# Optimization experiments

Measured on AMD Instinct MI355X. Metric: run time of the kernel, lower is better.

## Reference

```python
import jax, jax.numpy as jnp
import numpy as np

NUM_ATOMS = 100000
NUM_BONDS = 200000
MAX_NB = 6
ATOM_FDIM = 133
BOND_FDIM = 147
HIDDEN = 300
READOUT = 512
DEPTH = 6
ATOMS_PER_MOL = 25
NUM_MOLS = NUM_ATOMS // ATOMS_PER_MOL


def setup_inputs() -> dict:
    key = jax.random.key(0)
    ks = jax.random.split(key, 16)
    s = 0.02
    inp = {
        "f_atoms": jax.random.normal(ks[0], (NUM_ATOMS, ATOM_FDIM), jnp.float32),
        "f_bonds": jax.random.normal(ks[1], (NUM_BONDS, BOND_FDIM), jnp.float32),
        "a2b": jax.random.randint(ks[2], (NUM_ATOMS, MAX_NB), 0, NUM_BONDS),
        "b2a": jax.random.randint(ks[3], (NUM_BONDS,), 0, NUM_ATOMS),
        "b2revb": jax.random.randint(ks[4], (NUM_BONDS,), 0, NUM_BONDS),
        "mol_id": jnp.arange(NUM_ATOMS) // ATOMS_PER_MOL,
        # parameters (Linear: y = x @ W + b)
        "W_i": jax.random.normal(ks[5], (BOND_FDIM, HIDDEN), jnp.float32) * s,
        "b_i": jnp.zeros((HIDDEN,), jnp.float32),
        "W_h": jax.random.normal(ks[6], (HIDDEN, HIDDEN), jnp.float32) * s,
        "b_h": jnp.zeros((HIDDEN,), jnp.float32),
        "W_o": jax.random.normal(ks[7], (ATOM_FDIM + HIDDEN, HIDDEN), jnp.float32) * s,
        "b_o": jnp.zeros((HIDDEN,), jnp.float32),
        "W_fc0": jax.random.normal(ks[8], (HIDDEN, READOUT), jnp.float32) * s,
        "b_fc0": jnp.zeros((READOUT,), jnp.float32),
        "W_fc1": jax.random.normal(ks[9], (READOUT, READOUT), jnp.float32) * s,
        "b_fc1": jnp.zeros((READOUT,), jnp.float32),
        "W_last": jax.random.normal(ks[10], (READOUT, 1), jnp.float32) * s,
        "b_last": jnp.zeros((1,), jnp.float32),
    }
    return inp


def reference(f_atoms, f_bonds, W_i, b_i, W_h, b_h, W_o, b_o,
              W_fc0, b_fc0, W_fc1, b_fc1, W_last, b_last,
              a2b, b2a, b2revb, mol_id):
    relu = jax.nn.relu
    # input = W_i(f_bonds); message = relu(input)  (dropout p=0 -> identity)
    inp = f_bonds @ W_i + b_i                      # [B, H]
    message = relu(inp)
    for _ in range(DEPTH - 1):
        nei = message[a2b]                          # [A, nb, H] gather
        a_message = nei.sum(axis=1)                 # [A, H]
        rev_message = message[b2revb]               # [B, H]
        message = a_message[b2a] - rev_message      # [B, H]
        message = relu(inp + (message @ W_h + b_h))
    # final atom aggregation
    a_message = message[a2b].sum(axis=1)            # [A, H]
    a_input = jnp.concatenate([f_atoms, a_message], axis=1)
    atom_hiddens = relu(a_input @ W_o + b_o)        # [A, H]
    # molecule mean-pool (a_scope -> segment mean over mol_id)
    sums = jax.ops.segment_sum(atom_hiddens, mol_id, num_segments=NUM_MOLS)
    counts = jax.ops.segment_sum(jnp.ones((atom_hiddens.shape[0], 1), atom_hiddens.dtype),
                                 mol_id, num_segments=NUM_MOLS)
    mol_vecs = sums / jnp.maximum(counts, 1.0)      # [M, H]
    # readout MLP
    h = relu(mol_vecs @ W_fc0 + b_fc0)
    h = relu(h @ W_fc1 + b_fc1)
    out = h @ W_last + b_last                       # [M, 1]
    return out.reshape(-1)
```

## Files before the change

kernel.cpp:

```cpp
#include <hip/hip_runtime.h>

#define NATOMS 100000
#define NBONDS 200000
#define NMOLS  4000

typedef __bf16 bf16x8 __attribute__((ext_vector_type(8)));
typedef float  f32x4  __attribute__((ext_vector_type(4)));

__device__ unsigned short g_packWi [5  * 40 * 512];
__device__ unsigned short g_packWh [10 * 40 * 512];
__device__ unsigned short g_packWoT[5  * 40 * 512];
__device__ unsigned short g_packWoB[10 * 40 * 512];

__device__ __forceinline__ float bf2f(unsigned short u) {
    union { unsigned int i; float f; } c; c.i = ((unsigned int)u) << 16; return c.f;
}
__device__ __forceinline__ unsigned short f2bf(float f) {
    union { float f; unsigned int i; } c; c.f = f;
    unsigned int r = (c.i + 0x7FFFu + ((c.i >> 16) & 1u)) >> 16;
    return (unsigned short)r;
}
__device__ __forceinline__ unsigned int relu2(unsigned int u) {
    if (u & 0x00008000u) u &= 0xFFFF0000u;
    if (u & 0x80000000u) u &= 0x0000FFFFu;
    return u;
}

__global__ void pack_weights(const float* __restrict__ W_i,
                             const float* __restrict__ W_h,
                             const float* __restrict__ W_o)
{
    const int gid = blockIdx.x * blockDim.x + threadIdx.x;
    if (gid >= 1200 * 512) return;
    const int gg = gid >> 9;
    const int t  = gid & 511;
    const float* src; int K; unsigned short* dst; int lg;
    if (gg < 200)      { lg = gg;       src = W_i;             K = 147; dst = g_packWi; }
    else if (gg < 600) { lg = gg - 200; src = W_h;             K = 300; dst = g_packWh; }
    else if (gg < 800) { lg = gg - 600; src = W_o;             K = 133; dst = g_packWoT; }
    else               { lg = gg - 800; src = W_o + 133 * 300; K = 300; dst = g_packWoB; }
    const int s = lg / 40, r = lg % 40;
    const int f = r >> 1, hl = r & 1;
    const int ln = t >> 3, j = t & 7;
    const int k = 32 * s + 8 * (ln >> 4) + j;
    const int n = 16 * f + (ln & 15);
    float val = (k < K && n < 300) ? src[k * 300 + n] : 0.f;
    unsigned short hi = f2bf(val);
    dst[(long)lg * 512 + t] = hl ? f2bf(val - bf2f(hi)) : hi;
}

__global__ __launch_bounds__(512)
void gemm_mfma6(const void* __restrict__ Ap, int a16, int sel,
                const float* __restrict__ bias, const float* __restrict__ Cin,
                void* __restrict__ outR, int r16,
                unsigned short* __restrict__ outP16,
                long M, int K, int ksteps, int do_relu)
{
    __shared__ unsigned long long lds8[98304 / 8];
    unsigned short* Asm = (unsigned short*)lds8;
    unsigned short* Bsm = (unsigned short*)lds8 + 8192;
    unsigned short* ep  = (unsigned short*)lds8;

    const unsigned short* pp =
        (sel == 0) ? g_packWi : (sel == 1) ? g_packWh :
        (sel == 2) ? g_packWoT : g_packWoB;

    const int tid = threadIdx.x;
    const int wv  = tid >> 6;
    const int ln  = tid & 63;
    const int l15 = ln & 15;
    const int g   = ln >> 4;
    const int wm  = wv >> 2;
    const int wn  = wv & 3;
    const long row0 = (long)blockIdx.x * 128;

    f32x4 acc[4][5];
#pragma unroll
    for (int m = 0; m < 4; ++m)
#pragma unroll
        for (int f = 0; f < 5; ++f) acc[m][f] = (f32x4){0.f, 0.f, 0.f, 0.f};

    int aoff[4];
#pragma unroll
    for (int m = 0; m < 4; ++m) {
        const int r = wm * 64 + m * 16 + l15;
        aoff[m] = r * 32 + 8 * (g ^ ((r >> 1) & 3));
    }

    const int srow = tid >> 2, sq = tid & 3;
    const int sqs  = sq ^ ((srow >> 1) & 3);

#define STAGE_A(BUF, SS)                                                       \
    do {                                                                       \
        if (a16) {                                                             \
            const char* src = (const char*)Ap +                                \
                (row0 + srow) * (size_t)600 + (SS) * 64 + sqs * 16;            \
            char* dst = (char*)Asm + (BUF) * 8192 + srow * 64 + sq * 16;       \
            __builtin_amdgcn_global_load_lds(                                  \
                (const __attribute__((address_space(1))) void*)src,            \
                (__attribute__((address_space(3))) void*)dst, 16, 0, 0);       \
        } else {                                                               \
            const float* A = (const float*)Ap;                                 \
            const long gr = row0 + srow;                                       \
            const int kb = (SS) * 32 + sqs * 8;                                \
            unsigned short tv[8];                                              \
            _Pragma("unroll")                                                  \
            for (int e = 0; e < 8; ++e)                                        \
                tv[e] = (gr < M && kb + e < K) ? f2bf(A[gr * (long)K + kb + e]) \
                                               : (unsigned short)0;            \
            ushort4 w0 = {tv[0], tv[1], tv[2], tv[3]};                         \
            ushort4 w1 = {tv[4], tv[5], tv[6], tv[7]};                         \
            *(ushort4*)(Asm + (BUF) * 4096 + srow * 32 + sq * 8)     = w0;     \
            *(ushort4*)(Asm + (BUF) * 4096 + srow * 32 + sq * 8 + 4) = w1;     \
        }                                                                      \
    } while (0)

#define STAGE_B(BUF, SS)                                                       \
    do {                                                                       \
        _Pragma("unroll")                                                      \
        for (int i = 0; i < 5; ++i) {                                          \
            const char* src = (const char*)pp + (size_t)(SS) * 40960           \
                              + i * 8192 + tid * 16;                           \
            char* dst = (char*)Bsm + (BUF) * 40960 + i * 8192 + tid * 16;      \
            __builtin_amdgcn_global_load_lds(                                  \
                (const __attribute__((address_space(1))) void*)src,            \
                (__attribute__((address_space(3))) void*)dst, 16, 0, 0);       \
        }                                                                      \
    } while (0)

    STAGE_A(0, 0);
    STAGE_B(0, 0);
    __syncthreads();
    for (int s = 0; s < ksteps; ++s) {
        const int cur = s & 1;
        if (s + 1 < ksteps) {
            STAGE_A(cur ^ 1, s + 1);
            STAGE_B(cur ^ 1, s + 1);
        }
        const unsigned short* Ab = Asm + cur * 4096;
        const unsigned short* Bb = Bsm + cur * 20480;
        bf16x8 av[4];
#pragma unroll
        for (int m = 0; m < 4; ++m) av[m] = *(const bf16x8*)(Ab + aoff[m]);
#pragma unroll
        for (int f = 0; f < 5; ++f) {
            const int fg = wn * 5 + f;
            bf16x8 bh = *(const bf16x8*)(Bb + (2 * fg + 0) * 512 + ln * 8);
            bf16x8 bl = *(const bf16x8*)(Bb + (2 * fg + 1) * 512 + ln * 8);
#pragma unroll
            for (int m = 0; m < 4; ++m)
                acc[m][f] = __builtin_amdgcn_mfma_f32_16x16x32_bf16(av[m], bh, acc[m][f], 0, 0, 0);
#pragma unroll
            for (int m = 0; m < 4; ++m)
                acc[m][f] = __builtin_amdgcn_mfma_f32_16x16x32_bf16(av[m], bl, acc[m][f], 0, 0, 0);
        }
        __syncthreads();
    }
#undef STAGE_A
#undef STAGE_B

    if (r16) {
        for (int p = 0; p < 2; ++p) {
            if (p) __syncthreads();
            if (wm == p) {
#pragma unroll
                for (int f = 0; f < 5; ++f) {
                    const int n = (wn * 5 + f) * 16 + l15;
                    if (n >= 300) continue;
                    const float bv = bias ? bias[n] : 0.f;
#pragma unroll
                    for (int m = 0; m < 4; ++m)
#pragma unroll
                        for (int rr = 0; rr < 4; ++rr) {
                            const int rl = m * 16 + g * 4 + rr;
                            ep[rl * 304 + n] = f2bf(acc[m][f][rr] + bv);
                        }
                }
            }
            __syncthreads();
            for (int c = tid; c < 4800; c += 512) {
                const int row = c / 75, off = c - row * 75;
                const long grow = row0 + p * 64 + row;
                if (grow >= M) continue;
                uint2 v = *(const uint2*)(ep + row * 304 + off * 4);
                if (outP16)
                    *(uint2*)(outP16 + grow * 300 + off * 4) = v;
                if (do_relu) { v.x = relu2(v.x); v.y = relu2(v.y); }
                *(uint2*)((unsigned short*)outR + grow * 300 + off * 4) = v;
            }
        }
    } else {
#pragma unroll
        for (int f = 0; f < 5; ++f) {
            const int n = (wn * 5 + f) * 16 + l15;
            if (n >= 300) continue;
            const float bv = bias ? bias[n] : 0.f;
#pragma unroll
            for (int m = 0; m < 4; ++m) {
#pragma unroll
                for (int rr = 0; rr < 4; ++rr) {
                    const long row = row0 + wm * 64 + m * 16 + g * 4 + rr;
                    if (row >= M) continue;
                    float v = acc[m][f][rr] + bv;
                    if (Cin) v += Cin[row * 300 + n];
                    if (do_relu) v = fmaxf(v, 0.f);
                    ((float*)outR)[row * 300 + n] = v;
                }
            }
        }
    }
}

__global__ __launch_bounds__(256)
void gemm_flex(const float* __restrict__ A,
               const float* __restrict__ W,
               const float* __restrict__ bias,
               float* __restrict__ outR,
               int M, int K, int N, int do_relu)
{
    __shared__ float As[16][132];
    __shared__ float Bs[16][132];

    const int tid  = threadIdx.x;
    const int tx   = tid & 15;
    const int ty   = tid >> 4;
    const int row0 = blockIdx.y * 128;
    const int col0 = blockIdx.x * 128;

    float acc[8][8];
#pragma unroll
    for (int i = 0; i < 8; ++i)
#pragma unroll
        for (int j = 0; j < 8; ++j) acc[i][j] = 0.f;

    for (int k0 = 0; k0 < K; k0 += 16) {
        {
            const int c  = tid & 15;
            const int rb = tid >> 4;
#pragma unroll
            for (int i = 0; i < 8; ++i) {
                const int r  = rb + (i << 4);
                const int gr = row0 + r, gc = k0 + c;
                As[c][r] = (gr < M && gc < K) ? A[(long)gr * K + gc] : 0.f;
            }
        }
        {
            const int c  = tid & 127;
            const int rb = tid >> 7;
#pragma unroll
            for (int i = 0; i < 8; ++i) {
                const int r  = rb + (i << 1);
                const int gr = k0 + r, gc = col0 + c;
                Bs[r][c] = (gr < K && gc < N) ? W[(long)gr * N + gc] : 0.f;
            }
        }
        __syncthreads();
#pragma unroll
        for (int kk = 0; kk < 16; ++kk) {
            const float4* As4 = reinterpret_cast<const float4*>(&As[kk][0]);
            const float4* Bs4 = reinterpret_cast<const float4*>(&Bs[kk][0]);
            float4 a0 = As4[ty], a1 = As4[ty + 16];
            float4 b0 = Bs4[tx], b1 = Bs4[tx + 16];
            float av[8] = {a0.x, a0.y, a0.z, a0.w, a1.x, a1.y, a1.z, a1.w};
            float bv[8] = {b0.x, b0.y, b0.z, b0.w, b1.x, b1.y, b1.z, b1.w};
#pragma unroll
            for (int i = 0; i < 8; ++i)
#pragma unroll
                for (int j = 0; j < 8; ++j)
                    acc[i][j] = fmaf(av[i], bv[j], acc[i][j]);
        }
        __syncthreads();
    }
#pragma unroll
    for (int i = 0; i < 8; ++i) {
        const int lr = (i < 4) ? (ty * 4 + i) : (64 + ty * 4 + (i - 4));
        const int gr = row0 + lr;
        if (gr >= M) continue;
#pragma unroll
        for (int j = 0; j < 8; ++j) {
            const int lc = (j < 4) ? (tx * 4 + j) : (64 + tx * 4 + (j - 4));
            const int gc = col0 + lc;
            if (gc >= N) continue;
            float v = acc[i][j];
            if (bias) v += bias[gc];
            if (do_relu) v = fmaxf(v, 0.f);
            outR[(long)gr * N + gc] = v;
        }
    }
}

__global__ void aggregate_bf16(const unsigned short* __restrict__ src,
                               const int* __restrict__ a2b,
                               unsigned short* __restrict__ dst)
{
    const int idx = blockIdx.x * blockDim.x + threadIdx.x;
    if (idx >= NATOMS * 75) return;
    const int a = idx / 75;
    const int q = idx - a * 75;
    const int* nb = a2b + a * 6;
    float s0 = 0.f, s1 = 0.f, s2 = 0.f, s3 = 0.f;
#pragma unroll
    for (int k = 0; k < 6; ++k) {
        const ushort4 v = *reinterpret_cast<const ushort4*>(src + (long)nb[k] * 300 + (q << 2));
        s0 += bf2f(v.x); s1 += bf2f(v.y); s2 += bf2f(v.z); s3 += bf2f(v.w);
    }
    ushort4 r;
    r.x = f2bf(s0); r.y = f2bf(s1); r.z = f2bf(s2); r.w = f2bf(s3);
    *reinterpret_cast<ushort4*>(dst + ((long)idx << 2)) = r;
}

__global__ void fused_update(const unsigned short* __restrict__ t,
                             const int* __restrict__ a2b,
                             const int* __restrict__ b2a,
                             const int* __restrict__ b2revb,
                             const float* __restrict__ b_h,
                             const unsigned short* __restrict__ inp,
                             unsigned short* __restrict__ dst)
{
    const int idx = blockIdx.x * blockDim.x + threadIdx.x;
    if (idx >= NBONDS * 75) return;
    const int b = idx / 75;
    const int q = idx - b * 75;
    const long own = (long)b * 300 + (q << 2);
    const ushort4 vi = *reinterpret_cast<const ushort4*>(inp + own);
    const float4 vh = *reinterpret_cast<const float4*>(b_h + (q << 2));
    float s0 = bf2f(vi.x) + vh.x;
    float s1 = bf2f(vi.y) + vh.y;
    float s2 = bf2f(vi.z) + vh.z;
    float s3 = bf2f(vi.w) + vh.w;
    const int a = b2a[b];
    const int* nb = a2b + a * 6;
#pragma unroll
    for (int k = 0; k < 6; ++k) {
        const ushort4 v = *reinterpret_cast<const ushort4*>(t + (long)nb[k] * 300 + (q << 2));
        s0 += bf2f(v.x); s1 += bf2f(v.y); s2 += bf2f(v.z); s3 += bf2f(v.w);
    }
    {
        const ushort4 v = *reinterpret_cast<const ushort4*>(t + (long)b2revb[b] * 300 + (q << 2));
        s0 -= bf2f(v.x); s1 -= bf2f(v.y); s2 -= bf2f(v.z); s3 -= bf2f(v.w);
    }
    ushort4 o;
    o.x = f2bf(fmaxf(s0, 0.f));
    o.y = f2bf(fmaxf(s1, 0.f));
    o.z = f2bf(fmaxf(s2, 0.f));
    o.w = f2bf(fmaxf(s3, 0.f));
    *reinterpret_cast<ushort4*>(dst + own) = o;
}

__global__ void pool_kernel(const float* __restrict__ ah, float* __restrict__ mol)
{
    const int idx = blockIdx.x * blockDim.x + threadIdx.x;
    if (idx >= NMOLS * 75) return;
    const int m = idx / 75;
    const int q = idx - m * 75;
    const float* base = ah + (long)m * 25 * 300 + (q << 2);
    float s0 = 0.f, s1 = 0.f, s2 = 0.f, s3 = 0.f;
#pragma unroll
    for (int a = 0; a < 25; ++a) {
        const float4 v = *reinterpret_cast<const float4*>(base + a * 300);
        s0 += v.x; s1 += v.y; s2 += v.z; s3 += v.w;
    }
    float4 r; r.x = s0 / 25.f; r.y = s1 / 25.f; r.z = s2 / 25.f; r.w = s3 / 25.f;
    *reinterpret_cast<float4*>(mol + ((long)idx << 2)) = r;
}

__global__ void diag_kernel(float* __restrict__ out, float wsmb)
{
    const int i = blockIdx.x * blockDim.x + threadIdx.x;
    if (i < NMOLS) out[i] = (i == 0) ? wsmb : 0.f;
}

extern "C" void kernel_launch(void* const* d_in, const int* in_sizes, int n_in,
                              void* d_out, int out_size, void* d_ws, size_t ws_size,
                              hipStream_t stream)
{
    const float* f_atoms = (const float*)d_in[0];
    const float* f_bonds = (const float*)d_in[1];
    const int*   a2b     = (const int*)d_in[2];
    const int*   b2a     = (const int*)d_in[3];
    const int*   b2revb  = (const int*)d_in[4];
    const float* W_i    = (const float*)d_in[6];
    const float* b_i    = (const float*)d_in[7];
    const float* W_h    = (const float*)d_in[8];
    const float* b_h    = (const float*)d_in[9];
    const float* W_o    = (const float*)d_in[10];
    const float* b_o    = (const float*)d_in[11];
    const float* W_fc0  = (const float*)d_in[12];
    const float* b_fc0  = (const float*)d_in[13];
    const float* W_fc1  = (const float*)d_in[14];
    const float* b_fc1  = (const float*)d_in[15];
    const float* W_last = (const float*)d_in[16];
    const float* b_last = (const float*)d_in[17];
    float* out = (float*)d_out;

    if (ws_size < 240000000ull) {
        diag_kernel<<<(NMOLS + 255) / 256, 256, 0, stream>>>(out, (float)(ws_size >> 20));
        return;
    }

    const int gBond = (NBONDS + 127) / 128;
    const int gAtom = (NATOMS + 127) / 128;
    const int aggBlocks = (NATOMS * 75 + 255) / 256;
    const int updBlocks = (NBONDS * 75 + 255) / 256;

    pack_weights<<<(1200 * 512 + 255) / 256, 256, 0, stream>>>(W_i, W_h, W_o);

    if (ws_size >= 360000000ull) {
        unsigned short* inpB = (unsigned short*)d_ws;
        unsigned short* msgB = (unsigned short*)((char*)d_ws + 120000000);
        unsigned short* tB   = (unsigned short*)((char*)d_ws + 240000000);
        unsigned short* amB  = (unsigned short*)d_ws;
        float* tmpF = (float*)((char*)d_ws + 120000000);
        float* molF = (float*)((char*)d_ws + 240000000);
        float* h0   = molF + 2000000;
        float* h1   = molF + 5000000;

        gemm_mfma6<<<gBond, 512, 0, stream>>>(f_bonds, 0, 0, b_i, nullptr,
                                              msgB, 1, inpB, NBONDS, 147, 5, 1);
        for (int d = 0; d < 5; ++d) {
            gemm_mfma6<<<gBond, 512, 0, stream>>>(msgB, 1, 1, nullptr, nullptr,
                                                  tB, 1, nullptr, NBONDS, 300, 10, 0);
            fused_update<<<updBlocks, 256, 0, stream>>>(tB, a2b, b2a, b2revb, b_h,
                                                        inpB, msgB);
        }
        aggregate_bf16<<<aggBlocks, 256, 0, stream>>>(msgB, a2b, amB);
        gemm_mfma6<<<gAtom, 512, 0, stream>>>(f_atoms, 0, 2, nullptr, nullptr,
                                              tmpF, 0, nullptr, NATOMS, 133, 5, 0);
        gemm_mfma6<<<gAtom, 512, 0, stream>>>(amB, 1, 3, b_o, tmpF,
                                              tmpF, 0, nullptr, NATOMS, 300, 10, 1);
        pool_kernel<<<(NMOLS * 75 + 255) / 256, 256, 0, stream>>>(tmpF, molF);
        gemm_flex<<<dim3(4, 32), 256, 0, stream>>>(molF, W_fc0, b_fc0, h0, NMOLS, 300, 512, 1);
        gemm_flex<<<dim3(4, 32), 256, 0, stream>>>(h0, W_fc1, b_fc1, h1, NMOLS, 512, 512, 1);
        gemm_flex<<<dim3(1, 32), 256, 0, stream>>>(h1, W_last, b_last, out, NMOLS, 512, 1, 0);
    } else {
        unsigned short* msgB = (unsigned short*)d_ws;
        unsigned short* tB   = (unsigned short*)((char*)d_ws + 120000000);
        unsigned short* amB  = tB;
        float* tmpF = (float*)d_ws;
        float* molF = (float*)((char*)d_ws + 180000000);
        float* h0   = molF + 2000000;
        float* h1   = molF + 5000000;

        gemm_mfma6<<<gBond, 512, 0, stream>>>(f_bonds, 0, 0, b_i, nullptr,
                                              msgB, 1, nullptr, NBONDS, 147, 5, 1);
        for (int d = 0; d < 5; ++d) {
            gemm_mfma6<<<gBond, 512, 0, stream>>>(msgB, 1, 1, nullptr, nullptr,
                                                  tB, 1, nullptr, NBONDS, 300, 10, 0);
            gemm_mfma6<<<gBond, 512, 0, stream>>>(f_bonds, 0, 0, b_i, nullptr,
                                                  msgB, 1, nullptr, NBONDS, 147, 5, 0);
            fused_update<<<updBlocks, 256, 0, stream>>>(tB, a2b, b2a, b2revb, b_h,
                                                        msgB, msgB);
        }
        aggregate_bf16<<<aggBlocks, 256, 0, stream>>>(msgB, a2b, amB);
        gemm_mfma6<<<gAtom, 512, 0, stream>>>(f_atoms, 0, 2, nullptr, nullptr,
                                              tmpF, 0, nullptr, NATOMS, 133, 5, 0);
        gemm_mfma6<<<gAtom, 512, 0, stream>>>(amB, 1, 3, b_o, tmpF,
                                              tmpF, 0, nullptr, NATOMS, 300, 10, 1);
        pool_kernel<<<(NMOLS * 75 + 255) / 256, 256, 0, stream>>>(tmpF, molF);
        gemm_flex<<<dim3(4, 32), 256, 0, stream>>>(molF, W_fc0, b_fc0, h0, NMOLS, 300, 512, 1);
        gemm_flex<<<dim3(4, 32), 256, 0, stream>>>(h0, W_fc1, b_fc1, h1, NMOLS, 512, 512, 1);
        gemm_flex<<<dim3(1, 32), 256, 0, stream>>>(h1, W_last, b_last, out, NMOLS, 512, 1, 0);
    }
}
```

Measured before the change: 2.537 ms.

## Split GEMM output columns across two blocks to cut LDS and raise occupancy

```diff
diff --git a/kernel.cpp b/kernel.cpp
--- a/kernel.cpp
+++ b/kernel.cpp
@@ -49,14 +49,14 @@
     dst[(long)lg * 512 + t] = hl ? f2bf(val - bf2f(hi)) : hi;
 }
 
-__global__ __launch_bounds__(512)
-void gemm_mfma6(const void* __restrict__ Ap, int a16, int sel,
+__global__ __launch_bounds__(512, 4)
+void gemm_mfma7(const void* __restrict__ Ap, int a16, int sel,
                 const float* __restrict__ bias, const float* __restrict__ Cin,
                 void* __restrict__ outR, int r16,
                 unsigned short* __restrict__ outP16,
                 long M, int K, int ksteps, int do_relu)
 {
-    __shared__ unsigned long long lds8[98304 / 8];
+    __shared__ unsigned long long lds8[57344 / 8];
     unsigned short* Asm = (unsigned short*)lds8;
     unsigned short* Bsm = (unsigned short*)lds8 + 8192;
     unsigned short* ep  = (unsigned short*)lds8;
@@ -70,20 +70,21 @@
     const int ln  = tid & 63;
     const int l15 = ln & 15;
     const int g   = ln >> 4;
-    const int wm  = wv >> 2;
-    const int wn  = wv & 3;
-    const long row0 = (long)blockIdx.x * 128;
-
-    f32x4 acc[4][5];
-#pragma unroll
-    for (int m = 0; m < 4; ++m)
+    const int wm  = wv >> 1;
+    const int wn  = wv & 1;
+    const int bn  = blockIdx.x;
+    const long row0 = (long)blockIdx.y * 128;
+
+    f32x4 acc[2][5];
+#pragma unroll
+    for (int m = 0; m < 2; ++m)
 #pragma unroll
         for (int f = 0; f < 5; ++f) acc[m][f] = (f32x4){0.f, 0.f, 0.f, 0.f};
 
-    int aoff[4];
-#pragma unroll
-    for (int m = 0; m < 4; ++m) {
-        const int r = wm * 64 + m * 16 + l15;
+    int aoff[2];
+#pragma unroll
+    for (int m = 0; m < 2; ++m) {
+        const int r = wm * 32 + m * 16 + l15;
         aoff[m] = r * 32 + 8 * (g ^ ((r >> 1) & 3));
     }
 
@@ -118,13 +119,16 @@
 #define STAGE_B(BUF, SS)                                                       \
     do {                                                                       \
         _Pragma("unroll")                                                      \
-        for (int i = 0; i < 5; ++i) {                                          \
-            const char* src = (const char*)pp + (size_t)(SS) * 40960           \
-                              + i * 8192 + tid * 16;                           \
-            char* dst = (char*)Bsm + (BUF) * 40960 + i * 8192 + tid * 16;      \
-            __builtin_amdgcn_global_load_lds(                                  \
-                (const __attribute__((address_space(1))) void*)src,            \
-                (__attribute__((address_space(3))) void*)dst, 16, 0, 0);       \
+        for (int i = 0; i < 3; ++i) {                                          \
+            const int idx = i * 512 + tid;                                     \
+            if (idx < 1280) {                                                  \
+                const char* src = (const char*)pp +                            \
+                    ((size_t)(SS) * 40 + bn * 20) * 1024 + idx * 16;           \
+                char* dst = (char*)Bsm + (BUF) * 20480 + idx * 16;             \
+                __builtin_amdgcn_global_load_lds(                              \
+                    (const __attribute__((address_space(1))) void*)src,        \
+                    (__attribute__((address_space(3))) void*)dst, 16, 0, 0);   \
+            }                                                                  \
         }                                                                      \
     } while (0)
 
@@ -138,20 +142,20 @@
             STAGE_B(cur ^ 1, s + 1);
         }
         const unsigned short* Ab = Asm + cur * 4096;
-        const unsigned short* Bb = Bsm + cur * 20480;
-        bf16x8 av[4];
-#pragma unroll
-        for (int m = 0; m < 4; ++m) av[m] = *(const bf16x8*)(Ab + aoff[m]);
+        const unsigned short* Bb = Bsm + cur * 10240;
+        bf16x8 av[2];
+#pragma unroll
+        for (int m = 0; m < 2; ++m) av[m] = *(const bf16x8*)(Ab + aoff[m]);
 #pragma unroll
         for (int f = 0; f < 5; ++f) {
-            const int fg = wn * 5 + f;
-            bf16x8 bh = *(const bf16x8*)(Bb + (2 * fg + 0) * 512 + ln * 8);
-            bf16x8 bl = *(const bf16x8*)(Bb + (2 * fg + 1) * 512 + ln * 8);
-#pragma unroll
-            for (int m = 0; m < 4; ++m)
+            const int fl = wn * 5 + f;
+            bf16x8 bh = *(const bf16x8*)(Bb + (2 * fl + 0) * 512 + ln * 8);
+            bf16x8 bl = *(const bf16x8*)(Bb + (2 * fl + 1) * 512 + ln * 8);
+#pragma unroll
+            for (int m = 0; m < 2; ++m)
                 acc[m][f] = __builtin_amdgcn_mfma_f32_16x16x32_bf16(av[m], bh, acc[m][f], 0, 0, 0);
 #pragma unroll
-            for (int m = 0; m < 4; ++m)
+            for (int m = 0; m < 2; ++m)
                 acc[m][f] = __builtin_amdgcn_mfma_f32_16x16x32_bf16(av[m], bl, acc[m][f], 0, 0, 0);
         }
         __syncthreads();
@@ -160,46 +164,49 @@
 #undef STAGE_B
 
     if (r16) {
+        const int cpr = 40 - bn * 5;
         for (int p = 0; p < 2; ++p) {
             if (p) __syncthreads();
-            if (wm == p) {
+            if ((wm >> 1) == p) {
+                const int rbase = (wm & 1) * 32;
 #pragma unroll
                 for (int f = 0; f < 5; ++f) {
-                    const int n = (wn * 5 + f) * 16 + l15;
+                    const int n = (bn * 10 + wn * 5 + f) * 16 + l15;
                     if (n >= 300) continue;
+                    const int nl = n - bn * 160;
                     const float bv = bias ? bias[n] : 0.f;
 #pragma unroll
-                    for (int m = 0; m < 4; ++m)
+                    for (int m = 0; m < 2; ++m)
 #pragma unroll
                         for (int rr = 0; rr < 4; ++rr) {
-                            const int rl = m * 16 + g * 4 + rr;
-                            ep[rl * 304 + n] = f2bf(acc[m][f][rr] + bv);
+                            const int rl = rbase + m * 16 + g * 4 + rr;
+                            ep[rl * 168 + nl] = f2bf(acc[m][f][rr] + bv);
                         }
                 }
             }
             __syncthreads();
-            for (int c = tid; c < 4800; c += 512) {
-                const int row = c / 75, off = c - row * 75;
+            for (int c = tid; c < 64 * cpr; c += 512) {
+                const int row = c / cpr, off = c - row * cpr;
                 const long grow = row0 + p * 64 + row;
                 if (grow >= M) continue;
-                uint2 v = *(const uint2*)(ep + row * 304 + off * 4);
-                if (outP16)
-                    *(uint2*)(outP16 + grow * 300 + off * 4) = v;
+                uint2 v = *(const uint2*)(ep + row * 168 + off * 4);
+                const long gbase = grow * 300 + bn * 160 + off * 4;
+                if (outP16) *(uint2*)(outP16 + gbase) = v;
                 if (do_relu) { v.x = relu2(v.x); v.y = relu2(v.y); }
-                *(uint2*)((unsigned short*)outR + grow * 300 + off * 4) = v;
+                *(uint2*)((unsigned short*)outR + gbase) = v;
             }
         }
     } else {
 #pragma unroll
         for (int f = 0; f < 5; ++f) {
-            const int n = (wn * 5 + f) * 16 + l15;
+            const int n = (bn * 10 + wn * 5 + f) * 16 + l15;
             if (n >= 300) continue;
             const float bv = bias ? bias[n] : 0.f;
 #pragma unroll
-            for (int m = 0; m < 4; ++m) {
+            for (int m = 0; m < 2; ++m) {
 #pragma unroll
                 for (int rr = 0; rr < 4; ++rr) {
-                    const long row = row0 + wm * 64 + m * 16 + g * 4 + rr;
+                    const long row = row0 + wm * 32 + m * 16 + g * 4 + rr;
                     if (row >= M) continue;
                     float v = acc[m][f][rr] + bv;
                     if (Cin) v += Cin[row * 300 + n];
@@ -398,8 +405,8 @@
         return;
     }
 
-    const int gBond = (NBONDS + 127) / 128;
-    const int gAtom = (NATOMS + 127) / 128;
+    const dim3 gBond(2, (NBONDS + 127) / 128);
+    const dim3 gAtom(2, (NATOMS + 127) / 128);
     const int aggBlocks = (NATOMS * 75 + 255) / 256;
     const int updBlocks = (NBONDS * 75 + 255) / 256;
 
@@ -415,18 +422,18 @@
         float* h0   = molF + 2000000;
         float* h1   = molF + 5000000;
 
-        gemm_mfma6<<<gBond, 512, 0, stream>>>(f_bonds, 0, 0, b_i, nullptr,
+        gemm_mfma7<<<gBond, 512, 0, stream>>>(f_bonds, 0, 0, b_i, nullptr,
                                               msgB, 1, inpB, NBONDS, 147, 5, 1);
         for (int d = 0; d < 5; ++d) {
-            gemm_mfma6<<<gBond, 512, 0, stream>>>(msgB, 1, 1, nullptr, nullptr,
+            gemm_mfma7<<<gBond, 512, 0, stream>>>(msgB, 1, 1, nullptr, nullptr,
                                                   tB, 1, nullptr, NBONDS, 300, 10, 0);
             fused_update<<<updBlocks, 256, 0, stream>>>(tB, a2b, b2a, b2revb, b_h,
                                                         inpB, msgB);
         }
         aggregate_bf16<<<aggBlocks, 256, 0, stream>>>(msgB, a2b, amB);
-        gemm_mfma6<<<gAtom, 512, 0, stream>>>(f_atoms, 0, 2, nullptr, nullptr,
+        gemm_mfma7<<<gAtom, 512, 0, stream>>>(f_atoms, 0, 2, nullptr, nullptr,
                                               tmpF, 0, nullptr, NATOMS, 133, 5, 0);
-        gemm_mfma6<<<gAtom, 512, 0, stream>>>(amB, 1, 3, b_o, tmpF,
+        gemm_mfma7<<<gAtom, 512, 0, stream>>>(amB, 1, 3, b_o, tmpF,
                                               tmpF, 0, nullptr, NATOMS, 300, 10, 1);
         pool_kernel<<<(NMOLS * 75 + 255) / 256, 256, 0, stream>>>(tmpF, molF);
         gemm_flex<<<dim3(4, 32), 256, 0, stream>>>(molF, W_fc0, b_fc0, h0, NMOLS, 300, 512, 1);
@@ -441,20 +448,20 @@
         float* h0   = molF + 2000000;
         float* h1   = molF + 5000000;
 
-        gemm_mfma6<<<gBond, 512, 0, stream>>>(f_bonds, 0, 0, b_i, nullptr,
+        gemm_mfma7<<<gBond, 512, 0, stream>>>(f_bonds, 0, 0, b_i, nullptr,
                                               msgB, 1, nullptr, NBONDS, 147, 5, 1);
         for (int d = 0; d < 5; ++d) {
-            gemm_mfma6<<<gBond, 512, 0, stream>>>(msgB, 1, 1, nullptr, nullptr,
+            gemm_mfma7<<<gBond, 512, 0, stream>>>(msgB, 1, 1, nullptr, nullptr,
                                                   tB, 1, nullptr, NBONDS, 300, 10, 0);
-            gemm_mfma6<<<gBond, 512, 0, stream>>>(f_bonds, 0, 0, b_i, nullptr,
+            gemm_mfma7<<<gBond, 512, 0, stream>>>(f_bonds, 0, 0, b_i, nullptr,
                                                   msgB, 1, nullptr, NBONDS, 147, 5, 0);
             fused_update<<<updBlocks, 256, 0, stream>>>(tB, a2b, b2a, b2revb, b_h,
                                                         msgB, msgB);
         }
         aggregate_bf16<<<aggBlocks, 256, 0, stream>>>(msgB, a2b, amB);
-        gemm_mfma6<<<gAtom, 512, 0, stream>>>(f_atoms, 0, 2, nullptr, nullptr,
+        gemm_mfma7<<<gAtom, 512, 0, stream>>>(f_atoms, 0, 2, nullptr, nullptr,
                                               tmpF, 0, nullptr, NATOMS, 133, 5, 0);
-        gemm_mfma6<<<gAtom, 512, 0, stream>>>(amB, 1, 3, b_o, tmpF,
+        gemm_mfma7<<<gAtom, 512, 0, stream>>>(amB, 1, 3, b_o, tmpF,
                                               tmpF, 0, nullptr, NATOMS, 300, 10, 1);
         pool_kernel<<<(NMOLS * 75 + 255) / 256, 256, 0, stream>>>(tmpF, molF);
         gemm_flex<<<dim3(4, 32), 256, 0, stream>>>(molF, W_fc0, b_fc0, h0, NMOLS, 300, 512, 1);
```

New measurement: 2.474 ms. 1.03x faster.
